# Performance work log

Hardware: AMD Instinct MI355X
Metric: run time of the kernel (lower is better)

The kernel has to match this reference:

```python
import jax, jax.numpy as jnp
import numpy as np

H, DH = 16, 64  # n_head, head_dim


def setup_inputs() -> dict:
    key = jax.random.key(0)
    ks = jax.random.split(key, 14)
    B, L, D = 2, 1024, 1024
    d = DH

    def lin_w(k, fan_in, shape):
        return jax.random.normal(k, shape, jnp.float32) / np.sqrt(fan_in)

    return {
        "x": jax.random.normal(ks[0], (B, L, D), jnp.float32),
        "Wq": lin_w(ks[1], D, (D, D)),
        "bq": jnp.zeros((D,), jnp.float32),
        "Wk1": lin_w(ks[2], D, (D, D)),
        "bk1": jnp.zeros((D,), jnp.float32),
        "Wk2": lin_w(ks[3], D, (D, D)),
        "bk2": jnp.zeros((D,), jnp.float32),
        "Wg": lin_w(ks[4], d, (d, 1)),
        "bg": jnp.zeros((1,), jnp.float32),
        "Ws": lin_w(ks[5], d, (d, 1)),
        "bs": jnp.zeros((1,), jnp.float32),
        "Wp": lin_w(ks[6], D, (D, D)),
        "bp": jnp.zeros((D,), jnp.float32),
    }


def reference(x, Wq, bq, Wk1, bk1, Wk2, bk2, Wg, bg, Ws, bs, Wp, bp):
    B, L, D = x.shape
    d = DH
    # AR (GLA) branch
    Q = (x @ Wq + bq).reshape(B, L, H, d)
    K = (x @ Wk1 + bk1).reshape(B, L, H, d)
    V = x.reshape(B, L, H, d)
    W = jnp.einsum('blhd,blhe->blhde', K, V)  # (B,L,H,d,d) outer products
    # stable cumprod of sigmoid gate via log-cumsum-exp trick
    G = jax.nn.sigmoid(x.reshape(B, L, H, d) @ Wg + bg)            # (B,L,H,1)
    log_cum = jnp.clip(jnp.cumsum(jnp.log(jnp.clip(G, 1e-6, None)), axis=1), -30.0, 30.0)
    Gc = (jnp.exp(log_cum) + 1e-6)[..., None]                       # (B,L,H,1,1)
    R = jax.nn.silu(K @ Ws + bs)[..., None]                         # (B,L,H,1,1) decay gate
    Wc = jnp.cumsum(W * R / Gc, axis=1) * Gc                        # weighted cumsum
    O1 = jnp.einsum('blhd,blhde->blhe', Q, Wc)                      # (B,L,H,d)
    # MA branch on one-step residuals
    E = V[:, 1:] - O1[:, :-1]                                       # (B,L-1,H,d)
    q2 = -jax.nn.leaky_relu(-Q[:, :-1] / np.sqrt(d), 0.02)          # ma_q_activation (scale head_dim)
    k2 = jax.nn.sigmoid((x[:, :-1] @ Wk2 + bk2) / np.sqrt(D) * 0.02)  # ma_k_activation (scale n_embd)
    k2 = k2.reshape(B, L - 1, H, d)
    W_ma = jnp.cumsum(jnp.einsum('blhd,blhe->blhde', k2, E), axis=1)
    O2 = jnp.einsum('blhd,blhde->blhe', q2, W_ma)
    O2 = jnp.concatenate([jnp.zeros_like(O2[:, :1]), O2], axis=1)   # shift: first MA output is 0
    O = (O1 + O2).reshape(B, L, D)
    return O @ Wp + bp
```

## Files before the change

### kernel.cpp

```cpp
#include <hip/hip_runtime.h>
#include <hip/hip_bf16.h>
#include <math.h>

#define B_  2
#define L_  1024
#define D_  1024
#define H_  16
#define DH_ 64
#define M_  (B_*L_)
#define CHUNK 64
#define NCH (L_/CHUNK)
#define PT 72
#define PS 76

#define KSCALE (0.02f/32.0f)

using bf16x8 = __attribute__((ext_vector_type(8))) short;
using f32x4  = __attribute__((ext_vector_type(4))) float;

__device__ __forceinline__ unsigned short bf16r(float f){
  union{float f; unsigned int u;} x; x.f = f;
  unsigned int r = x.u + 0x7FFF + ((x.u>>16)&1);
  return (unsigned short)(r>>16);
}
__device__ __forceinline__ float bf2f(unsigned short u){
  union{unsigned int u; float f;} x; x.u = ((unsigned int)u)<<16; return x.f;
}

__global__ __launch_bounds__(256) void f32_to_bf16(
  const float* __restrict__ src, unsigned short* __restrict__ dst, int n4)
{
  int i = blockIdx.x*256 + threadIdx.x;
  int stride = gridDim.x*256;
  for (; i < n4; i += stride){
    float4 v = ((const float4*)src)[i];
    ushort4 o;
    o.x = bf16r(v.x); o.y = bf16r(v.y); o.z = bf16r(v.z); o.w = bf16r(v.w);
    ((ushort4*)dst)[i] = o;
  }
}

__global__ __launch_bounds__(256) void convert_wt(
  const float* __restrict__ W0, const float* __restrict__ W1,
  const float* __restrict__ W2, const float* __restrict__ W3,
  unsigned short* __restrict__ T0, unsigned short* __restrict__ T1,
  unsigned short* __restrict__ T2, unsigned short* __restrict__ T3)
{
  int which = blockIdx.z;
  const float* W = which==0?W0: which==1?W1: which==2?W2: W3;
  unsigned short* T = which==0?T0: which==1?T1: which==2?T2: T3;
  __shared__ float tile[64][65];
  int kBase = blockIdx.x*64, nBase = blockIdx.y*64;
  #pragma unroll
  for (int i=0;i<16;i++){
    int idx = threadIdx.x + i*256;
    int r = idx>>6, c = idx&63;
    tile[r][c] = W[(size_t)(kBase+r)*D_ + nBase+c];
  }
  __syncthreads();
  #pragma unroll
  for (int i=0;i<16;i++){
    int idx = threadIdx.x + i*256;
    int n = idx>>6, k = idx&63;
    T[(size_t)(nBase+n)*D_ + kBase+k] = bf16r(tile[k][n]);
  }
}

__device__ __forceinline__ void gemm_core(
    const unsigned short* __restrict__ A, const unsigned short* __restrict__ Bt,
    const float* __restrict__ bias, float* __restrict__ C,
    unsigned short* __restrict__ Cbf, int epi,
    int rowBase, int colBase)
{
  __shared__ __align__(16) unsigned short As[128*32];
  __shared__ __align__(16) unsigned short Bs[64*32];
  int tid = threadIdx.x, w = tid>>6, l = tid&63;
  int lr = l&15, g4 = l>>4;
  f32x4 acc[2][4];
  #pragma unroll
  for (int mi=0;mi<2;mi++)
    #pragma unroll
    for (int ni=0;ni<4;ni++)
      acc[mi][ni] = (f32x4){0.f,0.f,0.f,0.f};

  for (int k0 = 0; k0 < D_; k0 += 32) {
    #pragma unroll
    for (int i=0;i<2;i++){
      int F = (w*2+i)*64 + l;
      int r = F>>2, c16 = F&3;
      int sc = c16 ^ ((r>>1)&3);
      const unsigned short* g = A + (size_t)(rowBase+r)*D_ + k0 + sc*8;
      __builtin_amdgcn_global_load_lds(
        (const __attribute__((address_space(1))) void*)g,
        (__attribute__((address_space(3))) void*)(As + (size_t)(w*2+i)*512), 16, 0, 0);
    }
    {
      int F = w*64 + l;
      int r = F>>2, c16 = F&3;
      int sc = c16 ^ ((r>>1)&3);
      const unsigned short* g = Bt + (size_t)(colBase+r)*D_ + k0 + sc*8;
      __builtin_amdgcn_global_load_lds(
        (const __attribute__((address_space(1))) void*)g,
        (__attribute__((address_space(3))) void*)(Bs + (size_t)w*512), 16, 0, 0);
    }
    __syncthreads();
    bf16x8 af[2], bfr[4];
    #pragma unroll
    for (int mi=0;mi<2;mi++){
      int row = w*32 + mi*16 + lr;
      af[mi] = *(const bf16x8*)(As + row*32 + ((g4 ^ ((row>>1)&3))*8));
    }
    #pragma unroll
    for (int ni=0;ni<4;ni++){
      int n = ni*16 + lr;
      bfr[ni] = *(const bf16x8*)(Bs + n*32 + ((g4 ^ ((n>>1)&3))*8));
    }
    #pragma unroll
    for (int mi=0;mi<2;mi++)
      #pragma unroll
      for (int ni=0;ni<4;ni++)
        acc[mi][ni] = __builtin_amdgcn_mfma_f32_16x16x32_bf16(af[mi], bfr[ni], acc[mi][ni], 0,0,0);
    __syncthreads();
  }

  #pragma unroll
  for (int mi=0;mi<2;mi++){
    #pragma unroll
    for (int ni=0;ni<4;ni++){
      int col = colBase + ni*16 + lr;
      float bv = bias[col];
      #pragma unroll
      for (int r=0;r<4;r++){
        int row = rowBase + w*32 + mi*16 + g4*4 + r;
        float v = acc[mi][ni][r] + bv;
        if (epi) v = 1.f/(1.f + expf(-v*KSCALE));
        C[(size_t)row*D_ + col] = v;
        if (Cbf) Cbf[(size_t)row*D_ + col] = bf16r(v);
      }
    }
  }
}

__global__ __launch_bounds__(256) void gemm3(
  const unsigned short* __restrict__ A,
  const unsigned short* __restrict__ T0, const unsigned short* __restrict__ T1,
  const unsigned short* __restrict__ T2,
  const float* __restrict__ b0, const float* __restrict__ b1, const float* __restrict__ b2,
  float* __restrict__ C0, float* __restrict__ C1, float* __restrict__ C2,
  unsigned short* __restrict__ F0, unsigned short* __restrict__ F1,
  unsigned short* __restrict__ F2)
{
  int z = blockIdx.z;
  const unsigned short* Bt = z==0?T0: z==1?T1: T2;
  const float* bias = z==0?b0: z==1?b1: b2;
  float* C = z==0?C0: z==1?C1: C2;
  unsigned short* F = z==0?F0: z==1?F1: F2;
  gemm_core(A, Bt, bias, C, F, z==2 ? 1 : 0, blockIdx.x*128, blockIdx.y*64);
}

__global__ __launch_bounds__(256) void gemm1(
  const unsigned short* __restrict__ A, const unsigned short* __restrict__ Bt,
  const float* __restrict__ bias, float* __restrict__ C)
{
  gemm_core(A, Bt, bias, C, nullptr, 0, blockIdx.x*128, blockIdx.y*64);
}

__global__ __launch_bounds__(256) void scalars_kernel(
  const float* __restrict__ X, const float* __restrict__ K,
  const float* __restrict__ Wg, const float* __restrict__ bg,
  const float* __restrict__ Ws, const float* __restrict__ bs,
  float* __restrict__ GL, float* __restrict__ RR)
{
  int item = blockIdx.x * 4 + (threadIdx.x >> 6);
  int ln = threadIdx.x & 63;
  int row = item >> 4;
  int h = item & 15;
  float xv = X[(size_t)row*D_ + h*64 + ln];
  float kv = K[(size_t)row*D_ + h*64 + ln];
  float gdot = xv * Wg[ln];
  float rdot = kv * Ws[ln];
  #pragma unroll
  for (int off = 32; off; off >>= 1) {
    gdot += __shfl_xor(gdot, off);
    rdot += __shfl_xor(rdot, off);
  }
  if (ln == 0) {
    float glogit = gdot + bg[0];
    float sg = 1.f/(1.f+expf(-glogit));
    sg = fmaxf(sg, 1e-6f);
    GL[item] = logf(sg);
    float rlogit = rdot + bs[0];
    RR[item] = rlogit / (1.f + expf(-rlogit));
  }
}

__global__ __launch_bounds__(256) void gl_scan(
  const float* __restrict__ GL, const float* __restrict__ RR,
  float* __restrict__ GC, float* __restrict__ CF)
{
  int bh = blockIdx.x * 4 + (threadIdx.x >> 6);
  int b = bh >> 4, h = bh & 15;
  int ln = threadIdx.x & 63;
  float carry = 0.f;
  for (int it = 0; it < 16; ++it) {
    int l = it*64 + ln;
    float x = GL[((size_t)(b*L_ + l))*H_ + h];
    #pragma unroll
    for (int off = 1; off < 64; off <<= 1) {
      float t = __shfl_up(x, off);
      if (ln >= off) x += t;
    }
    float tot = __shfl(x, 63);
    float cum = carry + x;
    carry += tot;
    float lc = fminf(fmaxf(cum, -30.f), 30.f);
    float gc = expf(lc) + 1e-6f;
    GC[(size_t)bh*L_ + l] = gc;
    CF[(size_t)bh*L_ + l] = RR[((size_t)(b*L_ + l))*H_ + h] / gc;
  }
}

__global__ __launch_bounds__(256) void ar_chunk_sum(
  const unsigned short* __restrict__ Kbf, const unsigned short* __restrict__ Xbf,
  const float* __restrict__ CF, float* __restrict__ CS)
{
  int bh = blockIdx.x, c = blockIdx.y;
  int b = bh >> 4, h = bh & 15;
  int row0 = b*L_ + c*CHUNK;
  __shared__ __align__(16) unsigned short kt_t[64*PT];
  __shared__ __align__(16) unsigned short cv_t[64*PT];
  __shared__ __align__(16) float uni[64*PS];
  __shared__ float cf_s[64];
  int tid = threadIdx.x;
  if (tid < 64) cf_s[tid] = CF[(size_t)bh*L_ + c*CHUNK + tid];
  __syncthreads();
  const unsigned short* kg = Kbf + (size_t)row0*D_ + h*64;
  const unsigned short* vg = Xbf + (size_t)row0*D_ + h*64;
  #pragma unroll
  for (int t=0;t<16;t++){
    int idx = tid + t*256;
    int j = idx>>6, d = idx&63;
    kt_t[d*PT + j] = kg[(size_t)j*D_ + d];
    cv_t[d*PT + j] = bf16r(bf2f(vg[(size_t)j*D_ + d]) * cf_s[j]);
  }
  __syncthreads();
  int w = tid>>6, l = tid&63, lr = l&15, g4 = l>>4;
  f32x4 acc[4];
  #pragma unroll
  for (int ni=0;ni<4;ni++) acc[ni] = (f32x4){0.f,0.f,0.f,0.f};
  #pragma unroll
  for (int kk=0;kk<2;kk++){
    bf16x8 a = *(const bf16x8*)&cv_t[(w*16+lr)*PT + kk*32 + g4*8];
    #pragma unroll
    for (int ni=0;ni<4;ni++){
      bf16x8 bb = *(const bf16x8*)&kt_t[(ni*16+lr)*PT + kk*32 + g4*8];
      acc[ni] = __builtin_amdgcn_mfma_f32_16x16x32_bf16(a, bb, acc[ni], 0,0,0);
    }
  }
  #pragma unroll
  for (int ni=0;ni<4;ni++)
    #pragma unroll
    for (int r=0;r<4;r++)
      uni[(w*16+g4*4+r)*PS + ni*16+lr] = acc[ni][r];
  __syncthreads();
  float* out = CS + ((size_t)bh*NCH + c)*4096;
  #pragma unroll
  for (int t=0;t<4;t++){
    int idx = tid + t*256;
    int r = idx>>4, s = idx&15;
    *(float4*)&out[r*64 + s*4] = *(float4*)&uni[r*PS + s*4];
  }
}

__global__ __launch_bounds__(256) void ma_chunk_sum(
  const unsigned short* __restrict__ K2bf, const float* __restrict__ X,
  const float* __restrict__ O1, float* __restrict__ CS)
{
  int bh = blockIdx.x, c = blockIdx.y;
  int b = bh >> 4, h = bh & 15;
  int row0 = b*L_ + c*CHUNK;
  __shared__ __align__(16) unsigned short kt_t[64*PT];
  __shared__ __align__(16) unsigned short et_t[64*PT];
  __shared__ __align__(16) float uni[64*PS];
  int tid = threadIdx.x;
  const unsigned short* kg = K2bf + (size_t)row0*D_ + h*64;
  #pragma unroll
  for (int t=0;t<16;t++){
    int idx = tid + t*256;
    int j = idx>>6, d = idx&63;
    kt_t[d*PT + j] = kg[(size_t)j*D_ + d];
    float ev = 0.f;
    if (c*CHUNK + j < L_-1)
      ev = X[(size_t)(row0+j+1)*D_ + h*64 + d] - O1[(size_t)(row0+j)*D_ + h*64 + d];
    et_t[d*PT + j] = bf16r(ev);
  }
  __syncthreads();
  int w = tid>>6, l = tid&63, lr = l&15, g4 = l>>4;
  f32x4 acc[4];
  #pragma unroll
  for (int ni=0;ni<4;ni++) acc[ni] = (f32x4){0.f,0.f,0.f,0.f};
  #pragma unroll
  for (int kk=0;kk<2;kk++){
    bf16x8 a = *(const bf16x8*)&et_t[(w*16+lr)*PT + kk*32 + g4*8];
    #pragma unroll
    for (int ni=0;ni<4;ni++){
      bf16x8 bb = *(const bf16x8*)&kt_t[(ni*16+lr)*PT + kk*32 + g4*8];
      acc[ni] = __builtin_amdgcn_mfma_f32_16x16x32_bf16(a, bb, acc[ni], 0,0,0);
    }
  }
  #pragma unroll
  for (int ni=0;ni<4;ni++)
    #pragma unroll
    for (int r=0;r<4;r++)
      uni[(w*16+g4*4+r)*PS + ni*16+lr] = acc[ni][r];
  __syncthreads();
  float* out = CS + ((size_t)bh*NCH + c)*4096;
  #pragma unroll
  for (int t=0;t<4;t++){
    int idx = tid + t*256;
    int r = idx>>4, s = idx&15;
    *(float4*)&out[r*64 + s*4] = *(float4*)&uni[r*PS + s*4];
  }
}

__global__ __launch_bounds__(256) void scan_chunks_par(float* __restrict__ CS)
{
  int bh = blockIdx.x;
  int idx = blockIdx.y*256 + threadIdx.x;
  float run = 0.f;
  float* base = CS + (size_t)bh*NCH*4096 + idx;
  #pragma unroll
  for (int c = 0; c < NCH; ++c) {
    float cur = base[c*4096];
    base[c*4096] = run;
    run += cur;
  }
}

__global__ __launch_bounds__(256) void ar_o1_mfma(
  const unsigned short* __restrict__ Qbf, const unsigned short* __restrict__ Kbf,
  const unsigned short* __restrict__ Xbf, const float* __restrict__ CF,
  const float* __restrict__ GC, const float* __restrict__ CS,
  float* __restrict__ O1)
{
  int bh = blockIdx.x, c = blockIdx.y;
  int b = bh >> 4, h = bh & 15;
  int row0 = b*L_ + c*CHUNK;
  __shared__ __align__(16) unsigned short q_t[64*PT];
  __shared__ __align__(16) unsigned short k_t[64*PT];
  __shared__ __align__(16) unsigned short vt_t[64*PT];
  __shared__ __align__(16) unsigned short st_t[64*PT];
  __shared__ __align__(16) float uni[64*PS];
  unsigned short* p_t = (unsigned short*)uni;
  __shared__ float cf_s[64], gc_s[64];
  int tid = threadIdx.x;
  if (tid < 64) {
    cf_s[tid] = CF[(size_t)bh*L_ + c*CHUNK + tid];
    gc_s[tid] = GC[(size_t)bh*L_ + c*CHUNK + tid];
  }
  const unsigned short* qg = Qbf + (size_t)row0*D_ + h*64;
  const unsigned short* kg = Kbf + (size_t)row0*D_ + h*64;
  const unsigned short* vg = Xbf + (size_t)row0*D_ + h*64;
  const float* sg = CS + ((size_t)bh*NCH + c)*4096;
  #pragma unroll
  for (int t=0;t<2;t++){
    int idx = tid + t*256;
    int j = idx>>3, s = idx&7;
    *(uint4*)&q_t[j*PT + s*8] = *(const uint4*)&qg[(size_t)j*D_ + s*8];
    *(uint4*)&k_t[j*PT + s*8] = *(const uint4*)&kg[(size_t)j*D_ + s*8];
  }
  #pragma unroll
  for (int t=0;t<16;t++){
    int idx = tid + t*256;
    int j = idx>>6, d = idx&63;
    vt_t[d*PT + j] = vg[(size_t)j*D_ + d];
    st_t[j*PT + d] = bf16r(sg[idx]);
  }
  __syncthreads();
  int w = tid>>6, l = tid&63, lr = l&15, g4 = l>>4;
  f32x4 acc[4];
  #pragma unroll
  for (int ni=0;ni<4;ni++) acc[ni] = (f32x4){0.f,0.f,0.f,0.f};
  #pragma unroll
  for (int kk=0;kk<2;kk++){
    bf16x8 a = *(const bf16x8*)&q_t[(w*16+lr)*PT + kk*32 + g4*8];
    #pragma unroll
    for (int ni=0;ni<4;ni++){
      bf16x8 bb = *(const bf16x8*)&k_t[(ni*16+lr)*PT + kk*32 + g4*8];
      acc[ni] = __builtin_amdgcn_mfma_f32_16x16x32_bf16(a, bb, acc[ni], 0,0,0);
    }
  }
  #pragma unroll
  for (int ni=0;ni<4;ni++){
    int j = ni*16 + lr;
    float cf = cf_s[j];
    #pragma unroll
    for (int r=0;r<4;r++){
      int row = w*16 + g4*4 + r;
      float v = (j <= row) ? acc[ni][r]*cf : 0.f;
      p_t[row*PT + j] = bf16r(v);
    }
  }
  __syncthreads();
  #pragma unroll
  for (int ni=0;ni<4;ni++) acc[ni] = (f32x4){0.f,0.f,0.f,0.f};
  #pragma unroll
  for (int kk=0;kk<2;kk++){
    bf16x8 ap = *(const bf16x8*)&p_t[(w*16+lr)*PT + kk*32 + g4*8];
    bf16x8 aq = *(const bf16x8*)&q_t[(w*16+lr)*PT + kk*32 + g4*8];
    #pragma unroll
    for (int ni=0;ni<4;ni++){
      bf16x8 bv = *(const bf16x8*)&vt_t[(ni*16+lr)*PT + kk*32 + g4*8];
      bf16x8 bs = *(const bf16x8*)&st_t[(ni*16+lr)*PT + kk*32 + g4*8];
      acc[ni] = __builtin_amdgcn_mfma_f32_16x16x32_bf16(ap, bv, acc[ni], 0,0,0);
      acc[ni] = __builtin_amdgcn_mfma_f32_16x16x32_bf16(aq, bs, acc[ni], 0,0,0);
    }
  }
  __syncthreads();
  #pragma unroll
  for (int ni=0;ni<4;ni++)
    #pragma unroll
    for (int r=0;r<4;r++){
      int row = w*16 + g4*4 + r;
      uni[row*PS + ni*16 + lr] = gc_s[row]*acc[ni][r];
    }
  __syncthreads();
  #pragma unroll
  for (int t=0;t<4;t++){
    int idx = tid + t*256;
    int r = idx>>4, s = idx&15;
    *(float4*)&O1[(size_t)(row0+r)*D_ + h*64 + s*4] = *(float4*)&uni[r*PS + s*4];
  }
}

__global__ __launch_bounds__(256) void ma_o2_mfma(
  const unsigned short* __restrict__ Qbf, const unsigned short* __restrict__ K2bf,
  const float* __restrict__ X, const float* __restrict__ CS,
  float* __restrict__ O1)
{
  int bh = blockIdx.x, c = blockIdx.y;
  int b = bh >> 4, h = bh & 15;
  int row0 = b*L_ + c*CHUNK;
  __shared__ __align__(16) unsigned short q_t[64*PT];
  __shared__ __align__(16) unsigned short k_t[64*PT];
  __shared__ __align__(16) unsigned short et_t[64*PT];
  __shared__ __align__(16) unsigned short tt_t[64*PT];
  __shared__ __align__(16) float uni[64*PS];
  unsigned short* p_t = (unsigned short*)uni;
  int tid = threadIdx.x;
  const unsigned short* qg = Qbf  + (size_t)row0*D_ + h*64;
  const unsigned short* kg = K2bf + (size_t)row0*D_ + h*64;
  const float* sg = CS + ((size_t)bh*NCH + c)*4096;
  #pragma unroll
  for (int t=0;t<2;t++){
    int idx = tid + t*256;
    int j = idx>>3, s = idx&7;
    *(uint4*)&k_t[j*PT + s*8] = *(const uint4*)&kg[(size_t)j*D_ + s*8];
  }
  #pragma unroll
  for (int t=0;t<16;t++){
    int idx = tid + t*256;
    int j = idx>>6, d = idx&63;
    float qv = bf2f(qg[(size_t)j*D_ + d]);
    q_t[j*PT + d] = bf16r((qv > 0.f ? 0.02f*qv : qv) * 0.125f);
    float ev = 0.f;
    if (c*CHUNK + j < L_-1)
      ev = X[(size_t)(row0+j+1)*D_ + h*64 + d] - O1[(size_t)(row0+j)*D_ + h*64 + d];
    et_t[d*PT + j] = bf16r(ev);
    tt_t[j*PT + d] = bf16r(sg[idx]);
  }
  __syncthreads();
  int w = tid>>6, l = tid&63, lr = l&15, g4 = l>>4;
  f32x4 acc[4];
  #pragma unroll
  for (int ni=0;ni<4;ni++) acc[ni] = (f32x4){0.f,0.f,0.f,0.f};
  #pragma unroll
  for (int kk=0;kk<2;kk++){
    bf16x8 a = *(const bf16x8*)&q_t[(w*16+lr)*PT + kk*32 + g4*8];
    #pragma unroll
    for (int ni=0;ni<4;ni++){
      bf16x8 bb = *(const bf16x8*)&k_t[(ni*16+lr)*PT + kk*32 + g4*8];
      acc[ni] = __builtin_amdgcn_mfma_f32_16x16x32_bf16(a, bb, acc[ni], 0,0,0);
    }
  }
  #pragma unroll
  for (int ni=0;ni<4;ni++){
    int j = ni*16 + lr;
    #pragma unroll
    for (int r=0;r<4;r++){
      int row = w*16 + g4*4 + r;
      float v = (j <= row) ? acc[ni][r] : 0.f;
      p_t[row*PT + j] = bf16r(v);
    }
  }
  __syncthreads();
  #pragma unroll
  for (int ni=0;ni<4;ni++) acc[ni] = (f32x4){0.f,0.f,0.f,0.f};
  #pragma unroll
  for (int kk=0;kk<2;kk++){
    bf16x8 ap = *(const bf16x8*)&p_t[(w*16+lr)*PT + kk*32 + g4*8];
    bf16x8 aq = *(const bf16x8*)&q_t[(w*16+lr)*PT + kk*32 + g4*8];
    #pragma unroll
    for (int ni=0;ni<4;ni++){
      bf16x8 be = *(const bf16x8*)&et_t[(ni*16+lr)*PT + kk*32 + g4*8];
      bf16x8 bt = *(const bf16x8*)&tt_t[(ni*16+lr)*PT + kk*32 + g4*8];
      acc[ni] = __builtin_amdgcn_mfma_f32_16x16x32_bf16(ap, be, acc[ni], 0,0,0);
      acc[ni] = __builtin_amdgcn_mfma_f32_16x16x32_bf16(aq, bt, acc[ni], 0,0,0);
    }
  }
  __syncthreads();
  #pragma unroll
  for (int ni=0;ni<4;ni++)
    #pragma unroll
    for (int r=0;r<4;r++){
      int row = w*16 + g4*4 + r;
      uni[row*PS + ni*16 + lr] = acc[ni][r];
    }
  __syncthreads();
  #pragma unroll
  for (int t=0;t<4;t++){
    int idx = tid + t*256;
    int r = idx>>4, s = idx&15;
    if (c*CHUNK + r < L_-1) {
      float4* gp = (float4*)&O1[(size_t)(row0+r+1)*D_ + h*64 + s*4];
      float4 gv = *gp;
      float4 uv = *(float4*)&uni[r*PS + s*4];
      gv.x += uv.x; gv.y += uv.y; gv.z += uv.z; gv.w += uv.w;
      *gp = gv;
    }
  }
}

extern "C" void kernel_launch(void* const* d_in, const int* in_sizes, int n_in,
                              void* d_out, int out_size, void* d_ws, size_t ws_size,
                              hipStream_t stream) {
  const float* x  = (const float*)d_in[0];
  const float* Wq = (const float*)d_in[1];
  const float* bq = (const float*)d_in[2];
  const float* Wk1= (const float*)d_in[3];
  const float* bk1= (const float*)d_in[4];
  const float* Wk2= (const float*)d_in[5];
  const float* bk2= (const float*)d_in[6];
  const float* Wg = (const float*)d_in[7];
  const float* bg = (const float*)d_in[8];
  const float* Ws = (const float*)d_in[9];
  const float* bs = (const float*)d_in[10];
  const float* Wp = (const float*)d_in[11];
  const float* bp = (const float*)d_in[12];
  float* out = (float*)d_out;

  float* ws = (float*)d_ws;
  size_t MD = (size_t)M_*D_;
  float* Qb  = ws;
  float* Kb  = Qb  + MD;
  float* K2b = Kb  + MD;
  float* O1b = K2b + MD;
  float* CSb = O1b + MD;
  float* GLb = CSb + (size_t)32*NCH*4096;
  float* RRb = GLb + (size_t)M_*H_;
  float* GCb = RRb + (size_t)M_*H_;
  float* CFb = GCb + (size_t)32*L_;
  unsigned short* Xbf   = (unsigned short*)(CFb + (size_t)32*L_);
  unsigned short* Qbfs  = Xbf  + MD;
  unsigned short* Kbfs  = Qbfs + MD;
  unsigned short* K2bfs = Kbfs + MD;
  unsigned short* O1bf  = K2bfs+ MD;
  unsigned short* Wt0   = O1bf + MD;
  unsigned short* Wt1   = Wt0 + (size_t)D_*D_;
  unsigned short* Wt2   = Wt1 + (size_t)D_*D_;
  unsigned short* Wt3   = Wt2 + (size_t)D_*D_;

  f32_to_bf16<<<2048, 256, 0, stream>>>(x, Xbf, (int)(MD/4));
  dim3 gt(16, 16, 4);
  convert_wt<<<gt, 256, 0, stream>>>(Wq, Wk1, Wk2, Wp, Wt0, Wt1, Wt2, Wt3);

  dim3 gg(M_/128, D_/64, 3);
  gemm3<<<gg, 256, 0, stream>>>(Xbf, Wt0, Wt1, Wt2, bq, bk1, bk2,
                                Qb, Kb, K2b, Qbfs, Kbfs, K2bfs);

  scalars_kernel<<<(M_*H_)/4, 256, 0, stream>>>(x, Kb, Wg, bg, Ws, bs, GLb, RRb);
  gl_scan<<<8, 256, 0, stream>>>(GLb, RRb, GCb, CFb);

  dim3 gc(32, NCH);
  ar_chunk_sum<<<gc, 256, 0, stream>>>(Kbfs, Xbf, CFb, CSb);
  scan_chunks_par<<<gc, 256, 0, stream>>>(CSb);
  ar_o1_mfma<<<gc, 256, 0, stream>>>(Qbfs, Kbfs, Xbf, CFb, GCb, CSb, O1b);

  ma_chunk_sum<<<gc, 256, 0, stream>>>(K2bfs, x, O1b, CSb);
  scan_chunks_par<<<gc, 256, 0, stream>>>(CSb);
  ma_o2_mfma<<<gc, 256, 0, stream>>>(Qbfs, K2bfs, x, CSb, O1b);

  f32_to_bf16<<<2048, 256, 0, stream>>>(O1b, O1bf, (int)(MD/4));
  dim3 go(M_/128, D_/64);
  gemm1<<<go, 256, 0, stream>>>(O1bf, Wt3, bp, out);
}
```

Measured before the change: 201.6 us.

## Fold inter-chunk prefix scan into consumers and fuse O bf16 conversion

Removes the two scan_chunks_par launches. Each output block now sums all preceding chunk states itself (a prefix computed redundantly per block, up to 15 extra 16KB reads per block). ma_o2_mfma also writes the final O1+O2 directly as bf16 for the projection GEMM, which removes the separate f32_to_bf16 pass and the fp32 read-modify-write of O1. The trade is fewer launches and less memory traffic against quadratic redundant reads of the chunk states, which should mostly hit in cache.

```diff
diff --git a/kernel.cpp b/kernel.cpp
--- a/kernel.cpp
+++ b/kernel.cpp
@@ -320,20 +320,6 @@
     int idx = tid + t*256;
     int r = idx>>4, s = idx&15;
     *(float4*)&out[r*64 + s*4] = *(float4*)&uni[r*PS + s*4];
-  }
-}
-
-__global__ __launch_bounds__(256) void scan_chunks_par(float* __restrict__ CS)
-{
-  int bh = blockIdx.x;
-  int idx = blockIdx.y*256 + threadIdx.x;
-  float run = 0.f;
-  float* base = CS + (size_t)bh*NCH*4096 + idx;
-  #pragma unroll
-  for (int c = 0; c < NCH; ++c) {
-    float cur = base[c*4096];
-    base[c*4096] = run;
-    run += cur;
   }
 }
 
@@ -361,7 +347,14 @@
   const unsigned short* qg = Qbf + (size_t)row0*D_ + h*64;
   const unsigned short* kg = Kbf + (size_t)row0*D_ + h*64;
   const unsigned short* vg = Xbf + (size_t)row0*D_ + h*64;
-  const float* sg = CS + ((size_t)bh*NCH + c)*4096;
+  const float* csb = CS + (size_t)bh*NCH*4096;
+  float carry[16];
+  #pragma unroll
+  for (int i=0;i<16;i++) carry[i] = 0.f;
+  for (int c2=0;c2<c;c2++)
+    #pragma unroll
+    for (int i=0;i<16;i++)
+      carry[i] += csb[(size_t)c2*4096 + tid + i*256];
   #pragma unroll
   for (int t=0;t<2;t++){
     int idx = tid + t*256;
@@ -374,7 +367,11 @@
     int idx = tid + t*256;
     int j = idx>>6, d = idx&63;
     vt_t[d*PT + j] = vg[(size_t)j*D_ + d];
-    st_t[j*PT + d] = bf16r(sg[idx]);
+  }
+  #pragma unroll
+  for (int i=0;i<16;i++){
+    int idx = tid + i*256;
+    st_t[(idx>>6)*PT + (idx&63)] = bf16r(carry[i]);
   }
   __syncthreads();
   int w = tid>>6, l = tid&63, lr = l&15, g4 = l>>4;
@@ -436,7 +433,7 @@
 __global__ __launch_bounds__(256) void ma_o2_mfma(
   const unsigned short* __restrict__ Qbf, const unsigned short* __restrict__ K2bf,
   const float* __restrict__ X, const float* __restrict__ CS,
-  float* __restrict__ O1)
+  const float* __restrict__ O1, unsigned short* __restrict__ Obf)
 {
   int bh = blockIdx.x, c = blockIdx.y;
   int b = bh >> 4, h = bh & 15;
@@ -450,7 +447,14 @@
   int tid = threadIdx.x;
   const unsigned short* qg = Qbf  + (size_t)row0*D_ + h*64;
   const unsigned short* kg = K2bf + (size_t)row0*D_ + h*64;
-  const float* sg = CS + ((size_t)bh*NCH + c)*4096;
+  const float* csb = CS + (size_t)bh*NCH*4096;
+  float carry[16];
+  #pragma unroll
+  for (int i=0;i<16;i++) carry[i] = 0.f;
+  for (int c2=0;c2<c;c2++)
+    #pragma unroll
+    for (int i=0;i<16;i++)
+      carry[i] += csb[(size_t)c2*4096 + tid + i*256];
   #pragma unroll
   for (int t=0;t<2;t++){
     int idx = tid + t*256;
@@ -467,7 +471,11 @@
     if (c*CHUNK + j < L_-1)
       ev = X[(size_t)(row0+j+1)*D_ + h*64 + d] - O1[(size_t)(row0+j)*D_ + h*64 + d];
     et_t[d*PT + j] = bf16r(ev);
-    tt_t[j*PT + d] = bf16r(sg[idx]);
+  }
+  #pragma unroll
+  for (int i=0;i<16;i++){
+    int idx = tid + i*256;
+    tt_t[(idx>>6)*PT + (idx&63)] = bf16r(carry[i]);
   }
   __syncthreads();
   int w = tid>>6, l = tid&63, lr = l&15, g4 = l>>4;
@@ -522,12 +530,19 @@
     int idx = tid + t*256;
     int r = idx>>4, s = idx&15;
     if (c*CHUNK + r < L_-1) {
-      float4* gp = (float4*)&O1[(size_t)(row0+r+1)*D_ + h*64 + s*4];
-      float4 gv = *gp;
+      const float4 gv = *(const float4*)&O1[(size_t)(row0+r+1)*D_ + h*64 + s*4];
       float4 uv = *(float4*)&uni[r*PS + s*4];
-      gv.x += uv.x; gv.y += uv.y; gv.z += uv.z; gv.w += uv.w;
-      *gp = gv;
-    }
+      ushort4 o;
+      o.x = bf16r(gv.x+uv.x); o.y = bf16r(gv.y+uv.y);
+      o.z = bf16r(gv.z+uv.z); o.w = bf16r(gv.w+uv.w);
+      *(ushort4*)&Obf[(size_t)(row0+r+1)*D_ + h*64 + s*4] = o;
+    }
+  }
+  if (c == 0 && tid < 16) {
+    const float4 gv = *(const float4*)&O1[(size_t)row0*D_ + h*64 + tid*4];
+    ushort4 o;
+    o.x = bf16r(gv.x); o.y = bf16r(gv.y); o.z = bf16r(gv.z); o.w = bf16r(gv.w);
+    *(ushort4*)&Obf[(size_t)row0*D_ + h*64 + tid*4] = o;
   }
 }
 
@@ -564,8 +579,8 @@
   unsigned short* Qbfs  = Xbf  + MD;
   unsigned short* Kbfs  = Qbfs + MD;
   unsigned short* K2bfs = Kbfs + MD;
-  unsigned short* O1bf  = K2bfs+ MD;
-  unsigned short* Wt0   = O1bf + MD;
+  unsigned short* Obf   = K2bfs+ MD;
+  unsigned short* Wt0   = Obf + MD;
   unsigned short* Wt1   = Wt0 + (size_t)D_*D_;
   unsigned short* Wt2   = Wt1 + (size_t)D_*D_;
   unsigned short* Wt3   = Wt2 + (size_t)D_*D_;
@@ -583,14 +598,11 @@
 
   dim3 gc(32, NCH);
   ar_chunk_sum<<<gc, 256, 0, stream>>>(Kbfs, Xbf, CFb, CSb);
-  scan_chunks_par<<<gc, 256, 0, stream>>>(CSb);
   ar_o1_mfma<<<gc, 256, 0, stream>>>(Qbfs, Kbfs, Xbf, CFb, GCb, CSb, O1b);
 
   ma_chunk_sum<<<gc, 256, 0, stream>>>(K2bfs, x, O1b, CSb);
-  scan_chunks_par<<<gc, 256, 0, stream>>>(CSb);
-  ma_o2_mfma<<<gc, 256, 0, stream>>>(Qbfs, K2bfs, x, CSb, O1b);
-
-  f32_to_bf16<<<2048, 256, 0, stream>>>(O1b, O1bf, (int)(MD/4));
+  ma_o2_mfma<<<gc, 256, 0, stream>>>(Qbfs, K2bfs, x, CSb, O1b, Obf);
+
   dim3 go(M_/128, D_/64);
-  gemm1<<<go, 256, 0, stream>>>(O1bf, Wt3, bp, out);
-}
+  gemm1<<<go, 256, 0, stream>>>(Obf, Wt3, bp, out);
+}
```

Result: no change. 199.6 us (-1.0%).
